# Kernel tuning notes

Measured on AMD Instinct MI355X. Metric: run time of the kernel, lower is better.

The kernel has to match this reference:

```python
import jax, jax.numpy as jnp
import numpy as np

EPS = 1e-6
D = 512      # embedding_dim
M = 4        # n_modules
B = 4        # batch
S = 128      # seq_len
K = 32       # stack_size
STEPS = 16   # max_steps (ACT)
SCALE = D ** (-0.5)


def _clin(zr, zi, Wr, Wi, sub):
    # complex linear: (Wr + i Wi)(zr + i zi), torch Linear convention y = x @ W.T
    yr = jnp.einsum(sub, zr, Wr) - jnp.einsum(sub, zi, Wi)
    yi = jnp.einsum(sub, zi, Wr) + jnp.einsum(sub, zr, Wi)
    return yr, yi


def forward_fn(x_real, x_imag, Wl_r, Wl_i, Wq_r, Wq_i, Wk_r, Wk_i, Wv_r, Wv_i,
               ln_scale, ln_shift, mod_bias, gate_mask,
               score_w, score_b, conf_w, conf_b, halt_w, halt_b,
               ctrl_w, ctrl_b, st_score_w, st_score_b, st_conf_w, st_conf_b):
    mem0 = jnp.zeros((B, K, 2 * D), x_real.dtype)
    ptr0 = jnp.zeros((B, K), x_real.dtype).at[:, 0].set(1.0)
    acc0 = jnp.zeros((B, S, 2 * D), x_real.dtype)
    rem0 = jnp.ones((B,), x_real.dtype)

    def step(carry, _):
        sr, si, mem, ptr, acc, rem = carry
        # ComplexAttentionBlock (all M modules vectorized on axis m)
        cr = 0.5 * x_real + 0.5 * sr
        ci = 0.5 * x_imag + 0.5 * si
        zr, zi = _clin(cr, ci, Wl_r, Wl_i, 'bsd,mod->bmso')   # [B,M,S,D]
        # ComplexLayerNorm (magnitude LN, unbiased var as torch.var default)
        mag = jnp.sqrt(zr * zr + zi * zi) + EPS
        mean = mag.mean(-1, keepdims=True)
        var = mag.var(-1, keepdims=True, ddof=1)
        nm = (mag - mean) / jnp.sqrt(var + EPS)
        nm = nm * ln_scale[None, :, None, :] + ln_shift[None, :, None, :]
        ph = jnp.arctan2(zi, zr)
        zr = nm * jnp.cos(ph)
        zi = nm * jnp.sin(ph)
        # ModReLU
        nrm = jnp.sqrt(zr * zr + zi * zi) + EPS
        sc = jax.nn.relu(nrm + mod_bias[None, :, None, :]) / nrm
        zr = zr * sc
        zi = zi * sc
        # ComplexAttention over concatenated real/imag q,k
        sub = 'bmsd,mod->bmso'
        qr, qi = _clin(zr, zi, Wq_r, Wq_i, sub)
        kr, ki = _clin(zr, zi, Wk_r, Wk_i, sub)
        vr, vi = _clin(zr, zi, Wv_r, Wv_i, sub)
        qf = jnp.concatenate([qr, qi], -1)   # [B,M,S,2D]
        kf = jnp.concatenate([kr, ki], -1)
        attn = jax.nn.softmax(jnp.einsum('bmse,bmte->bmst', qf, kf) * SCALE, axis=-1)
        ar = jnp.einsum('bmst,bmtd->bmsd', attn, vr)
        ai = jnp.einsum('bmst,bmtd->bmsd', attn, vi)
        # SigmoidGatingMask
        g = jax.nn.sigmoid(gate_mask)[None, :, None, :]
        pr = ar * g
        pi = ai * g
        flat = jnp.concatenate([pr, pi], -1)  # [B,M,S,2D]
        score = jnp.einsum('bmse,me->bms', flat, score_w) + score_b[None, :, None]
        conf = jax.nn.sigmoid(jnp.einsum('bmse,me->bms', flat, conf_w) + conf_b[None, :, None])
        halt = jnp.einsum('bmse,me->bms', flat, halt_w) + halt_b[None, :, None]
        # DifferentiableStack on seq-pooled broadcast state
        flat_in = jnp.concatenate([sr.mean(1), si.mean(1)], -1)  # [B,2D]
        control = jax.nn.softmax(flat_in @ ctrl_w + ctrl_b, axis=-1)  # [B,3]
        push, pop, noop = control[:, 0:1], control[:, 1:2], control[:, 2:3]
        ptr_up = jnp.roll(ptr, 1, axis=1)
        ptr_dn = jnp.roll(ptr, -1, axis=1)
        new_ptr = push * ptr_up + pop * ptr_dn + noop * ptr
        new_ptr = new_ptr / (new_ptr.sum(1, keepdims=True) + EPS)
        wmask = push * ptr_up                                   # [B,K]
        new_mem = wmask[..., None] * flat_in[:, None, :] + mem * (1.0 - wmask[..., None])
        read = (new_mem * new_ptr[..., None]).sum(1)            # [B,2D]
        sp_r, sp_i = read[:, :D], read[:, D:]
        st_sc = read @ st_score_w + st_score_b[0]               # [B]
        st_cf = jax.nn.sigmoid(read @ st_conf_w + st_conf_b[0])
        # combine M block proposals + stack proposal via score*confidence softmax
        all_pr = jnp.concatenate([pr, jnp.broadcast_to(sp_r[:, None, None, :], (B, 1, S, D))], 1)
        all_pi = jnp.concatenate([pi, jnp.broadcast_to(sp_i[:, None, None, :], (B, 1, S, D))], 1)
        all_sc = jnp.concatenate([score, jnp.broadcast_to(st_sc[:, None, None], (B, 1, S))], 1)
        all_cf = jnp.concatenate([conf, jnp.broadcast_to(st_cf[:, None, None], (B, 1, S))], 1)
        w = jax.nn.softmax(all_sc * all_cf, axis=1)[..., None]  # [B,M+1,S,1]
        new_sr = (w * all_pr).sum(1)
        new_si = (w * all_pi).sum(1)
        # ACT halting accumulation
        p = jax.nn.sigmoid(halt).mean(axis=(1, 2))              # [B]
        acc = acc + (p * rem)[:, None, None] * jnp.concatenate([new_sr, new_si], -1)
        rem = rem * (1.0 - p)
        return (new_sr, new_si, new_mem, new_ptr, acc, rem), None

    carry, _ = jax.lax.scan(step, (x_real, x_imag, mem0, ptr0, acc0, rem0), None, length=STEPS)
    sr, si, _, _, acc, rem = carry
    # add ACT remainder weight on final state
    out = acc + rem[:, None, None] * jnp.concatenate([sr, si], -1)
    return out  # [B,S,2D] real/imag concat


def setup_inputs() -> dict:
    key = jax.random.key(0)
    ks = jax.random.split(key, 24)
    w = 1.0 / np.sqrt(D)
    h = 0.02
    inp = {
        'x_real': jax.random.normal(ks[0], (B, S, D), jnp.float32),
        'x_imag': jax.random.normal(ks[1], (B, S, D), jnp.float32),
        'Wl_r': jax.random.normal(ks[2], (M, D, D), jnp.float32) * w,
        'Wl_i': jax.random.normal(ks[3], (M, D, D), jnp.float32) * w,
        'Wq_r': jax.random.normal(ks[4], (M, D, D), jnp.float32) * w,
        'Wq_i': jax.random.normal(ks[5], (M, D, D), jnp.float32) * w,
        'Wk_r': jax.random.normal(ks[6], (M, D, D), jnp.float32) * w,
        'Wk_i': jax.random.normal(ks[7], (M, D, D), jnp.float32) * w,
        'Wv_r': jax.random.normal(ks[8], (M, D, D), jnp.float32) * w,
        'Wv_i': jax.random.normal(ks[9], (M, D, D), jnp.float32) * w,
        'ln_scale': jnp.ones((M, D), jnp.float32),
        'ln_shift': jnp.zeros((M, D), jnp.float32),
        'mod_bias': jnp.zeros((M, D), jnp.float32),
        'gate_mask': jnp.ones((M, D), jnp.float32),
        'score_w': jax.random.normal(ks[10], (M, 2 * D), jnp.float32) * h,
        'score_b': jnp.zeros((M,), jnp.float32),
        'conf_w': jax.random.normal(ks[11], (M, 2 * D), jnp.float32) * h,
        'conf_b': jnp.zeros((M,), jnp.float32),
        'halt_w': jax.random.normal(ks[12], (M, 2 * D), jnp.float32) * h,
        'halt_b': jnp.full((M,), -4.0, jnp.float32),  # nn.init.constant_(halt_head.bias, -4.0)
        'ctrl_w': jax.random.normal(ks[13], (2 * D, 3), jnp.float32) * h,
        'ctrl_b': jnp.zeros((3,), jnp.float32),
        'st_score_w': jax.random.normal(ks[14], (2 * D,), jnp.float32) * h,
        'st_score_b': jnp.zeros((1,), jnp.float32),
        'st_conf_w': jax.random.normal(ks[15], (2 * D,), jnp.float32) * h,
        'st_conf_b': jnp.zeros((1,), jnp.float32),
    }
    return inp


def reference(x_real, x_imag, Wl_r, Wl_i, Wq_r, Wq_i, Wk_r, Wk_i, Wv_r, Wv_i,
              ln_scale, ln_shift, mod_bias, gate_mask,
              score_w, score_b, conf_w, conf_b, halt_w, halt_b,
              ctrl_w, ctrl_b, st_score_w, st_score_b, st_conf_w, st_conf_b):
    return forward_fn(x_real, x_imag, Wl_r, Wl_i, Wq_r, Wq_i, Wk_r, Wk_i, Wv_r, Wv_i,
                      ln_scale, ln_shift, mod_bias, gate_mask,
                      score_w, score_b, conf_w, conf_b, halt_w, halt_b,
                      ctrl_w, ctrl_b, st_score_w, st_score_b, st_conf_w, st_conf_b)
```

## Files before the change

kernel.cpp:

```cpp
#include <hip/hip_runtime.h>

#define DD 512
#define MM 4
#define BB 4
#define SS 128
#define KK 32
#define NSTEPS 16
#define EPSF 1e-6f
#define SCALEF 0.04419417382415922f
#define BMSD (BB * MM * SS * DD)

typedef unsigned short u16;
typedef __bf16 bf16x8 __attribute__((ext_vector_type(8)));
typedef u16 u16x8 __attribute__((ext_vector_type(8)));
typedef float f32x16 __attribute__((ext_vector_type(16)));
typedef unsigned int u32x4 __attribute__((ext_vector_type(4)));

__device__ inline void split_bf16(float x, u16& h, u16& l) {
  __bf16 hb = (__bf16)x;
  float hf = (float)hb;
  __bf16 lb = (__bf16)(x - hf);
  h = __builtin_bit_cast(u16, hb);
  l = __builtin_bit_cast(u16, lb);
}

__global__ void k_convw(const float* __restrict__ src, u16* __restrict__ dst) {
  int idx = blockIdx.x * 256 + threadIdx.x;
  int row = idx >> 9, k = idx & 511;
  u16 h, l;
  split_bf16(src[idx], h, l);
  dst[(size_t)row * 1024 + k] = h;
  dst[(size_t)row * 1024 + 512 + k] = l;
}

__global__ void k_convt(const float* __restrict__ src, u16* __restrict__ dst) {
  __shared__ float tile[64][65];
  int m = blockIdx.z;
  int o0 = blockIdx.y * 64, d0 = blockIdx.x * 64;
  int tid = threadIdx.x;
  int g = tid >> 6, lane = tid & 63;
#pragma unroll
  for (int i = 0; i < 16; i++) {
    int o_l = g * 16 + i;
    tile[o_l][lane] = src[(size_t)(m * 512 + o0 + o_l) * 512 + d0 + lane];
  }
  __syncthreads();
#pragma unroll
  for (int i = 0; i < 16; i++) {
    int d_l = g * 16 + i;
    float v = tile[lane][d_l];
    u16 h, l;
    split_bf16(v, h, l);
    size_t drow = (size_t)(m * 512 + d0 + d_l) * 1024;
    dst[drow + o0 + lane] = h;
    dst[drow + 512 + o0 + lane] = l;
  }
}

__global__ void k_init(const float* __restrict__ xr, const float* __restrict__ xi,
                       float* __restrict__ sr, float* __restrict__ si,
                       float* __restrict__ acc, float* __restrict__ memv,
                       float* __restrict__ ptrv, float* __restrict__ rem,
                       u16* __restrict__ crbf, u16* __restrict__ cibf) {
  int idx = blockIdx.x * 256 + threadIdx.x;
  if (idx < BB * SS * 2 * DD) acc[idx] = 0.f;
  if (idx < BB * SS * DD) {
    float a = xr[idx], b = xi[idx];
    sr[idx] = a; si[idx] = b;
    int row = idx >> 9, d = idx & 511;
    u16 h, l;
    split_bf16(a, h, l);
    crbf[(size_t)row * 1024 + d] = h;
    crbf[(size_t)row * 1024 + 512 + d] = l;
    split_bf16(b, h, l);
    cibf[(size_t)row * 1024 + d] = h;
    cibf[(size_t)row * 1024 + 512 + d] = l;
  }
  if (idx < BB * KK * 2 * DD) memv[idx] = 0.f;
  if (idx < BB * KK) ptrv[idx] = ((idx & (KK - 1)) == 0) ? 1.f : 0.f;
  if (idx < BB) rem[idx] = 1.f;
}

__global__ void k_flatctrl(const float* __restrict__ sr, const float* __restrict__ si,
                           const float* __restrict__ ctrl_w, const float* __restrict__ ctrl_b,
                           float* __restrict__ ptrv, float* __restrict__ flat_in,
                           float* __restrict__ nptrg, float* __restrict__ wmg,
                           float* __restrict__ stacc,
                           float* __restrict__ scorev, float* __restrict__ confv,
                           float* __restrict__ haltv) {
  int b = blockIdx.x;
  int tid = threadIdx.x;
  __shared__ float red[3 * 256];
  __shared__ float ctrl[3], optr[KK], nptr_s[KK], wm_s[KK], normf;

  if (tid < KK) optr[tid] = ptrv[b * KK + tid];

#pragma unroll
  for (int i = 0; i < 2; i++) {
    int r = b * MM * SS + tid + i * 256;
    scorev[r] = 0.f; confv[r] = 0.f; haltv[r] = 0.f;
  }

  int e4 = tid * 4;
  const float* basep = (e4 < DD) ? sr : si;
  int d4 = (e4 < DD) ? e4 : (e4 - DD);
  float4 accv = make_float4(0.f, 0.f, 0.f, 0.f);
  size_t base = (size_t)b * SS * DD + d4;
  for (int s = 0; s < SS; s++) {
    float4 v = *(const float4*)&basep[base + (size_t)s * DD];
    accv.x += v.x; accv.y += v.y; accv.z += v.z; accv.w += v.w;
  }
  accv.x *= (1.0f / SS); accv.y *= (1.0f / SS); accv.z *= (1.0f / SS); accv.w *= (1.0f / SS);
  *(float4*)&flat_in[b * 2 * DD + e4] = accv;
  float fv[4] = {accv.x, accv.y, accv.z, accv.w};
  float d0 = 0.f, d1 = 0.f, d2 = 0.f;
#pragma unroll
  for (int j = 0; j < 4; j++) {
    d0 += fv[j] * ctrl_w[(e4 + j) * 3 + 0];
    d1 += fv[j] * ctrl_w[(e4 + j) * 3 + 1];
    d2 += fv[j] * ctrl_w[(e4 + j) * 3 + 2];
  }
  red[tid] = d0; red[256 + tid] = d1; red[512 + tid] = d2;
  __syncthreads();
  for (int off = 128; off > 0; off >>= 1) {
    if (tid < off) {
      red[tid] += red[tid + off];
      red[256 + tid] += red[256 + tid + off];
      red[512 + tid] += red[512 + tid + off];
    }
    __syncthreads();
  }
  if (tid == 0) {
    float l0 = red[0] + ctrl_b[0], l1 = red[256] + ctrl_b[1], l2 = red[512] + ctrl_b[2];
    float mx = fmaxf(l0, fmaxf(l1, l2));
    float e0 = expf(l0 - mx), e1 = expf(l1 - mx), e2 = expf(l2 - mx);
    float s = e0 + e1 + e2;
    ctrl[0] = e0 / s; ctrl[1] = e1 / s; ctrl[2] = e2 / s;
    stacc[b * 2] = 0.f; stacc[b * 2 + 1] = 0.f;
  }
  __syncthreads();
  if (tid < KK) {
    float up = optr[(tid + KK - 1) & (KK - 1)];
    float dn = optr[(tid + 1) & (KK - 1)];
    float cu = optr[tid];
    nptr_s[tid] = ctrl[0] * up + ctrl[1] * dn + ctrl[2] * cu;
    wm_s[tid] = ctrl[0] * up;
  }
  __syncthreads();
  if (tid == 0) {
    float s = 0.f;
    for (int k = 0; k < KK; k++) s += nptr_s[k];
    normf = 1.f / (s + EPSF);
  }
  __syncthreads();
  if (tid < KK) {
    float np = nptr_s[tid] * normf;
    ptrv[b * KK + tid] = np;
    nptrg[b * KK + tid] = np;
    wmg[b * KK + tid] = wm_s[tid];
  }
}

#define LSTR 72

__global__ __launch_bounds__(256) void k_gemm_mfma(
    const u16* __restrict__ Ar, const u16* __restrict__ Ai,
    const u16* __restrict__ Wr, const u16* __restrict__ Wi,
    float* __restrict__ Cr, float* __restrict__ Ci) {
  __shared__ u16 sAr[64][LSTR], sAi[64][LSTR], sWr[64][LSTR], sWi[64][LSTR];
  int mz = blockIdx.z;
  int m = mz & (MM - 1), split = mz >> 2;
  int row_blk = blockIdx.y * 64, o_blk = blockIdx.x * 64;
  int tid = threadIdx.x;

  int lrow = tid >> 3, lk8 = (tid & 7) << 3;
  size_t arow0 = (size_t)(row_blk + lrow), arow1 = arow0 + 32;
  size_t wrow0 = (size_t)m * DD + o_blk + lrow, wrow1 = wrow0 + 32;

  int wave = tid >> 6, lane = tid & 63;
  int wrow = (wave >> 1) * 32, wcol = (wave & 1) * 32;
  int l31 = lane & 31, khalf = (lane >> 5) * 8;

  f32x16 accP, accN, accI;
  for (int i = 0; i < 16; i++) { accP[i] = 0.f; accN[i] = 0.f; accI[i] = 0.f; }

  {
    int it2 = split, seg = it2 >> 3, k0 = (it2 & 7) * 64;
    int aofs = (seg == 1) ? 512 : 0, wofs = (seg == 2) ? 512 : 0;
    (void)aofs; (void)wofs;
  }
  int it20 = split;
  int seg0 = it20 >> 3, k00 = (it20 & 7) * 64;
  int aofs0 = (seg0 == 1) ? 512 : 0, wofs0 = (seg0 == 2) ? 512 : 0;
  u16x8 g0 = *(const u16x8*)&Ar[arow0 * 1024 + aofs0 + k00 + lk8];
  u16x8 g1 = *(const u16x8*)&Ar[arow1 * 1024 + aofs0 + k00 + lk8];
  u16x8 g2 = *(const u16x8*)&Ai[arow0 * 1024 + aofs0 + k00 + lk8];
  u16x8 g3 = *(const u16x8*)&Ai[arow1 * 1024 + aofs0 + k00 + lk8];
  u16x8 g4 = *(const u16x8*)&Wr[wrow0 * 1024 + wofs0 + k00 + lk8];
  u16x8 g5 = *(const u16x8*)&Wr[wrow1 * 1024 + wofs0 + k00 + lk8];
  u16x8 g6 = *(const u16x8*)&Wi[wrow0 * 1024 + wofs0 + k00 + lk8];
  u16x8 g7 = *(const u16x8*)&Wi[wrow1 * 1024 + wofs0 + k00 + lk8];

  for (int jt = 0; jt < 12; ++jt) {
    __syncthreads();
    *(u16x8*)&sAr[lrow][lk8] = g0;
    *(u16x8*)&sAr[lrow + 32][lk8] = g1;
    *(u16x8*)&sAi[lrow][lk8] = g2;
    *(u16x8*)&sAi[lrow + 32][lk8] = g3;
    *(u16x8*)&sWr[lrow][lk8] = g4;
    *(u16x8*)&sWr[lrow + 32][lk8] = g5;
    *(u16x8*)&sWi[lrow][lk8] = g6;
    *(u16x8*)&sWi[lrow + 32][lk8] = g7;
    u16x8 n0, n1, n2, n3, n4, n5, n6, n7;
    if (jt < 11) {
      int it2 = 2 * (jt + 1) + split, seg = it2 >> 3, k0 = (it2 & 7) * 64;
      int aofs = (seg == 1) ? 512 : 0, wofs = (seg == 2) ? 512 : 0;
      n0 = *(const u16x8*)&Ar[arow0 * 1024 + aofs + k0 + lk8];
      n1 = *(const u16x8*)&Ar[arow1 * 1024 + aofs + k0 + lk8];
      n2 = *(const u16x8*)&Ai[arow0 * 1024 + aofs + k0 + lk8];
      n3 = *(const u16x8*)&Ai[arow1 * 1024 + aofs + k0 + lk8];
      n4 = *(const u16x8*)&Wr[wrow0 * 1024 + wofs + k0 + lk8];
      n5 = *(const u16x8*)&Wr[wrow1 * 1024 + wofs + k0 + lk8];
      n6 = *(const u16x8*)&Wi[wrow0 * 1024 + wofs + k0 + lk8];
      n7 = *(const u16x8*)&Wi[wrow1 * 1024 + wofs + k0 + lk8];
    }
    __syncthreads();
#pragma unroll
    for (int kk = 0; kk < 64; kk += 16) {
      bf16x8 fAr = *(const bf16x8*)&sAr[wrow + l31][kk + khalf];
      bf16x8 fAi = *(const bf16x8*)&sAi[wrow + l31][kk + khalf];
      bf16x8 fWr = *(const bf16x8*)&sWr[wcol + l31][kk + khalf];
      bf16x8 fWi = *(const bf16x8*)&sWi[wcol + l31][kk + khalf];
      accP = __builtin_amdgcn_mfma_f32_32x32x16_bf16(fAr, fWr, accP, 0, 0, 0);
      accN = __builtin_amdgcn_mfma_f32_32x32x16_bf16(fAi, fWi, accN, 0, 0, 0);
      accI = __builtin_amdgcn_mfma_f32_32x32x16_bf16(fAi, fWr, accI, 0, 0, 0);
      accI = __builtin_amdgcn_mfma_f32_32x32x16_bf16(fAr, fWi, accI, 0, 0, 0);
    }
    if (jt < 11) {
      g0 = n0; g1 = n1; g2 = n2; g3 = n3; g4 = n4; g5 = n5; g6 = n6; g7 = n7;
    }
  }

  int o = o_blk + wcol + l31;
  size_t sofs = (size_t)split * BMSD;
#pragma unroll
  for (int reg = 0; reg < 16; reg++) {
    int r_in = (reg & 3) + 8 * (reg >> 2) + 4 * (lane >> 5);
    int gr = row_blk + wrow + r_in;
    int b = gr >> 7, s = gr & (SS - 1);
    size_t crow = (size_t)((b * MM + m) * SS + s);
    Cr[sofs + crow * DD + o] = accP[reg] - accN[reg];
    Ci[sofs + crow * DD + o] = accI[reg];
  }
}

__global__ __launch_bounds__(256) void k_gemm_g(
    const u16* __restrict__ Ar, const u16* __restrict__ Ai,
    const u16* __restrict__ Wr, const u16* __restrict__ Wi,
    float* __restrict__ Hr, float* __restrict__ Hi) {
  __shared__ u16 sAr[64][LSTR], sAi[64][LSTR], sWr[64][LSTR], sWi[64][LSTR];
  int m = blockIdx.z;
  int row_blk = blockIdx.y * 64, o_blk = blockIdx.x * 64;
  int tid = threadIdx.x;

  int lrow = tid >> 3, lk8 = (tid & 7) << 3;
  size_t arow0 = (size_t)(m * 512 + row_blk + lrow), arow1 = arow0 + 32;
  size_t wrow0 = (size_t)(m * 512 + o_blk + lrow), wrow1 = wrow0 + 32;

  int wave = tid >> 6, lane = tid & 63;
  int wrow = (wave >> 1) * 32, wcol = (wave & 1) * 32;
  int l31 = lane & 31, khalf = (lane >> 5) * 8;

  f32x16 accP, accN, accI;
  for (int i = 0; i < 16; i++) { accP[i] = 0.f; accN[i] = 0.f; accI[i] = 0.f; }

  u16x8 g0 = *(const u16x8*)&Ar[arow0 * 1024 + lk8];
  u16x8 g1 = *(const u16x8*)&Ar[arow1 * 1024 + lk8];
  u16x8 g2 = *(const u16x8*)&Ai[arow0 * 1024 + lk8];
  u16x8 g3 = *(const u16x8*)&Ai[arow1 * 1024 + lk8];
  u16x8 g4 = *(const u16x8*)&Wr[wrow0 * 1024 + lk8];
  u16x8 g5 = *(const u16x8*)&Wr[wrow1 * 1024 + lk8];
  u16x8 g6 = *(const u16x8*)&Wi[wrow0 * 1024 + lk8];
  u16x8 g7 = *(const u16x8*)&Wi[wrow1 * 1024 + lk8];

  for (int it = 0; it < 24; ++it) {
    __syncthreads();
    *(u16x8*)&sAr[lrow][lk8] = g0;
    *(u16x8*)&sAr[lrow + 32][lk8] = g1;
    *(u16x8*)&sAi[lrow][lk8] = g2;
    *(u16x8*)&sAi[lrow + 32][lk8] = g3;
    *(u16x8*)&sWr[lrow][lk8] = g4;
    *(u16x8*)&sWr[lrow + 32][lk8] = g5;
    *(u16x8*)&sWi[lrow][lk8] = g6;
    *(u16x8*)&sWi[lrow + 32][lk8] = g7;
    u16x8 n0, n1, n2, n3, n4, n5, n6, n7;
    if (it < 23) {
      int it2 = it + 1, seg = it2 >> 3, k0 = (it2 & 7) * 64;
      int aofs = (seg == 1) ? 512 : 0, wofs = (seg == 2) ? 512 : 0;
      n0 = *(const u16x8*)&Ar[arow0 * 1024 + aofs + k0 + lk8];
      n1 = *(const u16x8*)&Ar[arow1 * 1024 + aofs + k0 + lk8];
      n2 = *(const u16x8*)&Ai[arow0 * 1024 + aofs + k0 + lk8];
      n3 = *(const u16x8*)&Ai[arow1 * 1024 + aofs + k0 + lk8];
      n4 = *(const u16x8*)&Wr[wrow0 * 1024 + wofs + k0 + lk8];
      n5 = *(const u16x8*)&Wr[wrow1 * 1024 + wofs + k0 + lk8];
      n6 = *(const u16x8*)&Wi[wrow0 * 1024 + wofs + k0 + lk8];
      n7 = *(const u16x8*)&Wi[wrow1 * 1024 + wofs + k0 + lk8];
    }
    __syncthreads();
#pragma unroll
    for (int kk = 0; kk < 64; kk += 16) {
      bf16x8 fAr = *(const bf16x8*)&sAr[wrow + l31][kk + khalf];
      bf16x8 fAi = *(const bf16x8*)&sAi[wrow + l31][kk + khalf];
      bf16x8 fWr = *(const bf16x8*)&sWr[wcol + l31][kk + khalf];
      bf16x8 fWi = *(const bf16x8*)&sWi[wcol + l31][kk + khalf];
      u32x4 t = __builtin_bit_cast(u32x4, fAi) ^ 0x80008000u;
      bf16x8 nAi = __builtin_bit_cast(bf16x8, t);
      accP = __builtin_amdgcn_mfma_f32_32x32x16_bf16(fAr, fWr, accP, 0, 0, 0);
      accN = __builtin_amdgcn_mfma_f32_32x32x16_bf16(fAi, fWi, accN, 0, 0, 0);
      accI = __builtin_amdgcn_mfma_f32_32x32x16_bf16(fAr, fWi, accI, 0, 0, 0);
      accI = __builtin_amdgcn_mfma_f32_32x32x16_bf16(nAi, fWr, accI, 0, 0, 0);
    }
    if (it < 23) {
      g0 = n0; g1 = n1; g2 = n2; g3 = n3; g4 = n4; g5 = n5; g6 = n6; g7 = n7;
    }
  }

  int o = o_blk + wcol + l31;
#pragma unroll
  for (int reg = 0; reg < 16; reg++) {
    int r_in = (reg & 3) + 8 * (reg >> 2) + 4 * (lane >> 5);
    int gr = row_blk + wrow + r_in;
    size_t crow = (size_t)(m * 512 + gr);
    Hr[crow * DD + o] = accP[reg] + accN[reg];
    Hi[crow * DD + o] = accI[reg];
  }
}

__global__ __launch_bounds__(256) void k_gemm_qkv(
    const u16* __restrict__ Ar, const u16* __restrict__ Ai,
    const u16* __restrict__ wbf, size_t WSLOT,
    u16* __restrict__ qbr, u16* __restrict__ qbi,
    u16* __restrict__ vbr, u16* __restrict__ vbi) {
  __shared__ u16 sAr[64][LSTR], sAi[64][LSTR], sWr[64][LSTR], sWi[64][LSTR];
// ... 195 lines not shown
  sum += __shfl_xor(sum, 2);
  float inv = 1.f / sum;
  size_t prow = (size_t)(bm * SS + s_blk + row) * 256;
#pragma unroll
  for (int j = 0; j < 32; j++) {
    int c = quarter * 32 + j;
    u16 h, l;
    split_bf16(ev[j] * inv, h, l);
    Pb[prow + c] = h;
    Pb[prow + 128 + c] = l;
  }
}

__global__ __launch_bounds__(256) void k_pv(
    const u16* __restrict__ Pb, const u16* __restrict__ vbr, const u16* __restrict__ vbi,
    const float* __restrict__ gate_mask,
    const float* __restrict__ score_w, const float* __restrict__ conf_w,
    const float* __restrict__ halt_w,
    float* __restrict__ pr, float* __restrict__ pi,
    float* __restrict__ scorev, float* __restrict__ confv, float* __restrict__ haltv) {
  __shared__ u16 sP[64][LSTR], sVr[64][LSTR], sVi[64][LSTR];
  int bm = blockIdx.z;
  int m = bm & (MM - 1);
  int s_blk = blockIdx.y * 64;
  int o_blk = blockIdx.x * 64;
  int tid = threadIdx.x;
  int lrow = tid >> 3, lk8 = (tid & 7) << 3;
  size_t prow0 = (size_t)(bm * SS + s_blk + lrow), prow1 = prow0 + 32;

  int wave = tid >> 6, lane = tid & 63;
  int wrow = (wave >> 1) * 32;
  int wcol = (wave & 1) * 32;
  int l31 = lane & 31, khalf = (lane >> 5) * 8;

  f32x16 accR, accI;
  for (int i = 0; i < 16; i++) { accR[i] = 0.f; accI[i] = 0.f; }

  for (int it = 0; it < 6; ++it) {
    int seg = it >> 1, k0 = (it & 1) * 64;
    int pofs = (seg == 1) ? 128 : 0;
    int vofs = (seg == 2) ? 512 : 0;
    u16x8 p0 = *(const u16x8*)&Pb[prow0 * 256 + pofs + k0 + lk8];
    u16x8 p1 = *(const u16x8*)&Pb[prow1 * 256 + pofs + k0 + lk8];
    size_t vrow0 = (size_t)(bm * SS + k0 + lrow), vrow1 = vrow0 + 32;
    u16x8 v0 = *(const u16x8*)&vbr[vrow0 * 1024 + vofs + o_blk + lk8];
    u16x8 v1 = *(const u16x8*)&vbr[vrow1 * 1024 + vofs + o_blk + lk8];
    u16x8 w0 = *(const u16x8*)&vbi[vrow0 * 1024 + vofs + o_blk + lk8];
    u16x8 w1 = *(const u16x8*)&vbi[vrow1 * 1024 + vofs + o_blk + lk8];
    __syncthreads();
    *(u16x8*)&sP[lrow][lk8] = p0;
    *(u16x8*)&sP[lrow + 32][lk8] = p1;
    *(u16x8*)&sVr[lrow][lk8] = v0;
    *(u16x8*)&sVr[lrow + 32][lk8] = v1;
    *(u16x8*)&sVi[lrow][lk8] = w0;
    *(u16x8*)&sVi[lrow + 32][lk8] = w1;
    __syncthreads();
#pragma unroll
    for (int kk = 0; kk < 64; kk += 16) {
      bf16x8 fP = *(const bf16x8*)&sP[wrow + l31][kk + khalf];
      u16x8 ar, ai;
#pragma unroll
      for (int j = 0; j < 8; j++) {
        ar[j] = sVr[kk + khalf + j][wcol + l31];
        ai[j] = sVi[kk + khalf + j][wcol + l31];
      }
      accR = __builtin_amdgcn_mfma_f32_32x32x16_bf16(fP, __builtin_bit_cast(bf16x8, ar), accR, 0, 0, 0);
      accI = __builtin_amdgcn_mfma_f32_32x32x16_bf16(fP, __builtin_bit_cast(bf16x8, ai), accI, 0, 0, 0);
    }
  }

  int d = o_blk + wcol + l31;
  float g = 1.f / (1.f + expf(-gate_mask[m * DD + d]));
  float swr = score_w[m * 2 * DD + d], swi = score_w[m * 2 * DD + DD + d];
  float cwr = conf_w[m * 2 * DD + d],  cwi = conf_w[m * 2 * DD + DD + d];
  float hwr = halt_w[m * 2 * DD + d],  hwi = halt_w[m * 2 * DD + DD + d];
#pragma unroll
  for (int reg = 0; reg < 16; reg++) {
    int r_in = (reg & 3) + 8 * (reg >> 2) + 4 * (lane >> 5);
    size_t crow = (size_t)(bm * SS + s_blk + wrow + r_in);
    float vR = accR[reg] * g, vI = accI[reg] * g;
    pr[crow * DD + d] = vR;
    pi[crow * DD + d] = vI;
    float ps = vR * swr + vI * swi;
    float pc = vR * cwr + vI * cwi;
    float ph = vR * hwr + vI * hwi;
#pragma unroll
    for (int off = 1; off < 32; off <<= 1) {
      ps += __shfl_xor(ps, off);
      pc += __shfl_xor(pc, off);
      ph += __shfl_xor(ph, off);
    }
    if (l31 == 0) {
      atomicAdd(&scorev[crow], ps);
      atomicAdd(&confv[crow], pc);
      atomicAdd(&haltv[crow], ph);
    }
  }
}

__global__ void k_lnphase(const float* __restrict__ zr, const float* __restrict__ zi,
                          const float* __restrict__ ln_scale, const float* __restrict__ ln_shift,
                          const float* __restrict__ mod_bias,
                          u16* __restrict__ zbr, u16* __restrict__ zbi) {
  int row = blockIdx.x;
  int m = (row >> 7) & (MM - 1);
  int tid = threadIdx.x;
  size_t base = (size_t)row * DD;
  float zrv[4], ziv[4], rv[4];
  float sum = 0.f, sumsq = 0.f;
#pragma unroll
  for (int i = 0; i < 4; i++) {
    int o = tid + i * 128;
    float a = zr[base + o] + zr[(size_t)BMSD + base + o];
    float bv = zi[base + o] + zi[(size_t)BMSD + base + o];
    zrv[i] = a; ziv[i] = bv;
    float r = sqrtf(a * a + bv * bv);
    rv[i] = r;
    float mg = r + EPSF;
    sum += mg;
    sumsq += mg * mg;
  }
  __shared__ float rs[128], rq[128];
  rs[tid] = sum; rq[tid] = sumsq;
  __syncthreads();
  for (int off = 64; off > 0; off >>= 1) {
    if (tid < off) { rs[tid] += rs[tid + off]; rq[tid] += rq[tid + off]; }
    __syncthreads();
  }
  float mean = rs[0] * (1.0f / DD);
  float var = (rq[0] - (float)DD * mean * mean) * (1.0f / (DD - 1));
  float inv = 1.0f / sqrtf(var + EPSF);
#pragma unroll
  for (int i = 0; i < 4; i++) {
    int o = tid + i * 128;
    float mg = rv[i] + EPSF;
    float nm = (mg - mean) * inv * ln_scale[m * DD + o] + ln_shift[m * DD + o];
    float r = rv[i];
    float cosp, sinp;
    if (r > 0.f) { cosp = zrv[i] / r; sinp = ziv[i] / r; }
    else { cosp = 1.f; sinp = 0.f; }
    float z1r = nm * cosp, z1i = nm * sinp;
    float nrm = sqrtf(z1r * z1r + z1i * z1i) + EPSF;
    float sc = fmaxf(nrm + mod_bias[m * DD + o], 0.f) / nrm;
    u16 h, l;
    split_bf16(z1r * sc, h, l);
    zbr[(size_t)row * 1024 + o] = h;
    zbr[(size_t)row * 1024 + 512 + o] = l;
    split_bf16(z1i * sc, h, l);
    zbi[(size_t)row * 1024 + o] = h;
    zbi[(size_t)row * 1024 + 512 + o] = l;
  }
}

__global__ void k_memup(const float* __restrict__ flat_in,
                        const float* __restrict__ nptrg, const float* __restrict__ wmg,
                        float* __restrict__ memv, float* __restrict__ readv,
                        const float* __restrict__ st_score_w, const float* __restrict__ st_conf_w,
                        float* __restrict__ stacc) {
  int b = blockIdx.x >> 2;
  int chunk = blockIdx.x & 3;
  int tid = threadIdx.x;
  int e = chunk * 256 + tid;
  __shared__ float nptr[KK], wm[KK];
  __shared__ float red[256], red2[256];
  if (tid < KK) { nptr[tid] = nptrg[b * KK + tid]; wm[tid] = wmg[b * KK + tid]; }
  __syncthreads();
  float fl = flat_in[b * 2 * DD + e];
  float racc = 0.f;
#pragma unroll
  for (int k = 0; k < KK; k++) {
    size_t idx = ((size_t)(b * KK + k)) * 2 * DD + e;
    float nm = wm[k] * fl + memv[idx] * (1.f - wm[k]);
    memv[idx] = nm;
    racc += nm * nptr[k];
  }
  readv[b * 2 * DD + e] = racc;
  red[tid] = racc * st_score_w[e];
  red2[tid] = racc * st_conf_w[e];
  __syncthreads();
  for (int off = 128; off > 0; off >>= 1) {
    if (tid < off) { red[tid] += red[tid + off]; red2[tid] += red2[tid + off]; }
    __syncthreads();
  }
  if (tid == 0) {
    atomicAdd(&stacc[b * 2], red[0]);
    atomicAdd(&stacc[b * 2 + 1], red2[0]);
  }
}

__global__ void k_haltp(const float* __restrict__ halt, const float* __restrict__ halt_b,
                        float* __restrict__ rem,
                        float* __restrict__ coeff, const float* __restrict__ stacc,
                        const float* __restrict__ st_score_b, const float* __restrict__ st_conf_b,
                        float* __restrict__ stv) {
  int b = blockIdx.x;
  int tid = threadIdx.x;
  __shared__ float red[256];
  float v0 = halt[b * MM * SS + tid] + halt_b[tid >> 7];
  float v1 = halt[b * MM * SS + 256 + tid] + halt_b[(tid + 256) >> 7];
  red[tid] = 1.f / (1.f + expf(-v0)) + 1.f / (1.f + expf(-v1));
  __syncthreads();
  for (int off = 128; off > 0; off >>= 1) {
    if (tid < off) red[tid] += red[tid + off];
    __syncthreads();
  }
  if (tid == 0) {
    float p = red[0] * (1.0f / (MM * SS));
    float r = rem[b];
    coeff[b] = p * r;
    rem[b] = r * (1.f - p);
    stv[b] = stacc[b * 2] + st_score_b[0];
    stv[BB + b] = 1.f / (1.f + expf(-(stacc[b * 2 + 1] + st_conf_b[0])));
  }
}

__global__ void k_combine(const float* __restrict__ pr, const float* __restrict__ pi,
                          const float* __restrict__ score, const float* __restrict__ conf,
                          const float* __restrict__ score_b, const float* __restrict__ conf_b,
                          const float* __restrict__ stv, const float* __restrict__ readv,
                          const float* __restrict__ coeff,
                          const float* __restrict__ xr, const float* __restrict__ xi,
                          float* __restrict__ sr, float* __restrict__ si, float* __restrict__ acc,
                          u16* __restrict__ crbf, u16* __restrict__ cibf) {
  int bs = blockIdx.x;
  int b = bs >> 7, s = bs & (SS - 1);
  int tid = threadIdx.x;
  __shared__ float w[5];
  if (tid == 0) {
    float l[5];
    for (int m = 0; m < MM; m++) {
      int r = (b * MM + m) * SS + s;
      float sc = score[r] + score_b[m];
      float cf = 1.f / (1.f + expf(-(conf[r] + conf_b[m])));
      l[m] = sc * cf;
    }
    l[4] = stv[b] * stv[BB + b];
    float mx = l[0];
    for (int j = 1; j < 5; j++) mx = fmaxf(mx, l[j]);
    float sum = 0.f;
    for (int j = 0; j < 5; j++) { l[j] = expf(l[j] - mx); sum += l[j]; }
    for (int j = 0; j < 5; j++) w[j] = l[j] / sum;
  }
  __syncthreads();
  float cf = coeff[b];
#pragma unroll
  for (int i = 0; i < 2; i++) {
    int d = tid + i * 256;
    float nsr = w[4] * readv[b * 2 * DD + d];
    float nsi = w[4] * readv[b * 2 * DD + DD + d];
#pragma unroll
    for (int m = 0; m < MM; m++) {
      size_t off = ((size_t)((b * MM + m) * SS + s)) * DD + d;
      nsr += w[m] * pr[off];
      nsi += w[m] * pi[off];
    }
    size_t sidx = (size_t)bs * DD + d;
    sr[sidx] = nsr;
    si[sidx] = nsi;
    size_t aoff = (size_t)bs * 2 * DD;
    acc[aoff + d] += cf * nsr;
    acc[aoff + DD + d] += cf * nsi;
    u16 h, l;
    split_bf16(0.5f * xr[sidx] + 0.5f * nsr, h, l);
    crbf[(size_t)bs * 1024 + d] = h;
    crbf[(size_t)bs * 1024 + 512 + d] = l;
    split_bf16(0.5f * xi[sidx] + 0.5f * nsi, h, l);
    cibf[(size_t)bs * 1024 + d] = h;
    cibf[(size_t)bs * 1024 + 512 + d] = l;
  }
}

__global__ void k_final(const float* __restrict__ acc, const float* __restrict__ rem,
                        const float* __restrict__ sr, const float* __restrict__ si,
                        float* __restrict__ out) {
  int idx = blockIdx.x * 256 + threadIdx.x;
  int e = idx & (2 * DD - 1);
  int bs = idx >> 10;
  int b = bs >> 7;
  float v = (e < DD) ? sr[(size_t)bs * DD + e] : si[(size_t)bs * DD + e - DD];
  out[idx] = acc[idx] + rem[b] * v;
}

extern "C" void kernel_launch(void* const* d_in, const int* in_sizes, int n_in,
                              void* d_out, int out_size, void* d_ws, size_t ws_size,
                              hipStream_t stream) {
  const float* xr = (const float*)d_in[0];
  const float* xi = (const float*)d_in[1];
  const float* Wl_r = (const float*)d_in[2];
  const float* Wl_i = (const float*)d_in[3];
  const float* Wq_r = (const float*)d_in[4];
  const float* Wq_i = (const float*)d_in[5];
  const float* Wk_r = (const float*)d_in[6];
  const float* Wk_i = (const float*)d_in[7];
  const float* Wv_r = (const float*)d_in[8];
  const float* Wv_i = (const float*)d_in[9];
  const float* ln_scale = (const float*)d_in[10];
  const float* ln_shift = (const float*)d_in[11];
  const float* mod_bias = (const float*)d_in[12];
  const float* gate_mask = (const float*)d_in[13];
  const float* score_w = (const float*)d_in[14];
  const float* score_b = (const float*)d_in[15];
  const float* conf_w = (const float*)d_in[16];
  const float* conf_b = (const float*)d_in[17];
  const float* halt_w = (const float*)d_in[18];
  const float* halt_b = (const float*)d_in[19];
  const float* ctrl_w = (const float*)d_in[20];
  const float* ctrl_b = (const float*)d_in[21];
  const float* st_score_w = (const float*)d_in[22];
  const float* st_score_b = (const float*)d_in[23];
  const float* st_conf_w = (const float*)d_in[24];
  const float* st_conf_b = (const float*)d_in[25];
  float* out = (float*)d_out;

  const int BSD = BB * SS * DD;
  const size_t WSLOT = (size_t)MM * DD * 1024;

  char* pc = (char*)d_ws;
  float* sr = (float*)pc; pc += (size_t)BSD * 4;
  float* si = (float*)pc; pc += (size_t)BSD * 4;
  float* zr = (float*)pc; pc += (size_t)2 * BMSD * 4;
  float* zi = (float*)pc; pc += (size_t)2 * BMSD * 4;
  float* prb = (float*)pc; pc += (size_t)BMSD * 4;
  float* pib = (float*)pc; pc += (size_t)BMSD * 4;
  float* scorev = (float*)pc; pc += (size_t)BB * MM * SS * 4;
  float* confv = (float*)pc; pc += (size_t)BB * MM * SS * 4;
  float* haltv = (float*)pc; pc += (size_t)BB * MM * SS * 4;
  float* flat = (float*)pc; pc += (size_t)BB * 2 * DD * 4;
  float* stacc = (float*)pc; pc += 64;
  float* nptrg = (float*)pc; pc += (size_t)BB * KK * 4;
  float* wmg = (float*)pc; pc += (size_t)BB * KK * 4;
  float* memv = (float*)pc; pc += (size_t)BB * KK * 2 * DD * 4;
  float* ptrv = (float*)pc; pc += (size_t)BB * KK * 4;
  float* readv = (float*)pc; pc += (size_t)BB * 2 * DD * 4;
  float* stv = (float*)pc; pc += (size_t)2 * BB * 4;
  float* accb = (float*)pc; pc += (size_t)BB * SS * 2 * DD * 4;
  float* rem = (float*)pc; pc += (size_t)BB * 4;
  float* coeff = (float*)pc; pc += (size_t)BB * 4;
  u16* crbf = (u16*)pc; pc += (size_t)BB * SS * 1024 * 2;
  u16* cibf = (u16*)pc; pc += (size_t)BB * SS * 1024 * 2;
  u16* zbr = (u16*)pc; pc += (size_t)BB * MM * SS * 1024 * 2;
  u16* zbi = (u16*)pc; pc += (size_t)BB * MM * SS * 1024 * 2;
  u16* qbr = (u16*)pc; pc += (size_t)BB * MM * SS * 1024 * 2;
  u16* qbi = (u16*)pc; pc += (size_t)BB * MM * SS * 1024 * 2;
  u16* vbr = (u16*)pc; pc += (size_t)BB * MM * SS * 1024 * 2;
  u16* vbi = (u16*)pc; pc += (size_t)BB * MM * SS * 1024 * 2;
  u16* Pb  = (u16*)pc; pc += (size_t)BB * MM * SS * 256 * 2;
  u16* wbf = (u16*)pc; pc += 10 * WSLOT * 2;
  u16* wqtr = (u16*)pc; pc += WSLOT * 2;
  u16* wqti = (u16*)pc; pc += WSLOT * 2;
  u16* wktr = (u16*)pc; pc += WSLOT * 2;
  u16* wkti = (u16*)pc; pc += WSLOT * 2;
  float* hfr = (float*)pc; pc += (size_t)MM * DD * DD * 4;
  float* hfi = (float*)pc; pc += (size_t)MM * DD * DD * 4;

  k_convw<<<4096, 256, 0, stream>>>(Wl_r, wbf + 0 * WSLOT);
  k_convw<<<4096, 256, 0, stream>>>(Wl_i, wbf + 1 * WSLOT);
  k_convw<<<4096, 256, 0, stream>>>(Wv_r, wbf + 6 * WSLOT);
  k_convw<<<4096, 256, 0, stream>>>(Wv_i, wbf + 7 * WSLOT);

  dim3 tgrid(8, 8, 4);
  k_convt<<<tgrid, 256, 0, stream>>>(Wq_r, wqtr);
  k_convt<<<tgrid, 256, 0, stream>>>(Wq_i, wqti);
  k_convt<<<tgrid, 256, 0, stream>>>(Wk_r, wktr);
  k_convt<<<tgrid, 256, 0, stream>>>(Wk_i, wkti);

  dim3 hgrid(8, 8, 4);
  k_gemm_g<<<hgrid, 256, 0, stream>>>(wktr, wkti, wqtr, wqti, hfr, hfi);
  k_convw<<<4096, 256, 0, stream>>>(hfr, wbf + 8 * WSLOT);
  k_convw<<<4096, 256, 0, stream>>>(hfi, wbf + 9 * WSLOT);

  k_init<<<2048, 256, 0, stream>>>(xr, xi, sr, si, accb, memv, ptrv, rem, crbf, cibf);

  dim3 ggrid(DD / 64, (BB * SS) / 64, MM * 2);
  dim3 qgrid(DD / 64, (BB * SS) / 64, MM * 2);
  dim3 smgrid(1, SS / 64, BB * MM);
  dim3 pvgrid(DD / 64, SS / 64, BB * MM);

  for (int step = 0; step < NSTEPS; ++step) {
    k_flatctrl<<<BB, 256, 0, stream>>>(sr, si, ctrl_w, ctrl_b, ptrv, flat, nptrg, wmg, stacc,
                                       scorev, confv, haltv);
    k_gemm_mfma<<<ggrid, 256, 0, stream>>>(crbf, cibf, wbf + 0 * WSLOT, wbf + 1 * WSLOT, zr, zi);
    k_lnphase<<<BB * MM * SS, 128, 0, stream>>>(zr, zi, ln_scale, ln_shift, mod_bias, zbr, zbi);
    k_gemm_qkv<<<qgrid, 256, 0, stream>>>(zbr, zbi, wbf, WSLOT, qbr, qbi, vbr, vbi);
    k_scores_sm<<<smgrid, 256, 0, stream>>>(qbr, qbi, zbr, zbi, Pb);
    k_pv<<<pvgrid, 256, 0, stream>>>(Pb, vbr, vbi, gate_mask, score_w, conf_w, halt_w,
                                     prb, pib, scorev, confv, haltv);
    k_memup<<<BB * 4, 256, 0, stream>>>(flat, nptrg, wmg, memv, readv,
                                        st_score_w, st_conf_w, stacc);
    k_haltp<<<BB, 256, 0, stream>>>(haltv, halt_b, rem, coeff, stacc, st_score_b, st_conf_b, stv);
    k_combine<<<BB * SS, 256, 0, stream>>>(prb, pib, scorev, confv, score_b, conf_b,
                                           stv, readv, coeff,
                                           xr, xi, sr, si, accb, crbf, cibf);
  }

  k_final<<<(BB * SS * 2 * DD) / 256, 256, 0, stream>>>(accb, rem, sr, si, out);
}
```

Baseline: 2.186 ms.

## Fuse stack controller, memory update and halting into fewer per-step kernels

Merges the flat/controller kernel with the stack memory update into one 512-thread kernel, and folds the halting-probability reduction into the combine kernel using ping-pong remainder buffers. The sequence-mean 'flat' vector is now accumulated with atomics inside combine and init instead of being re-read from sr/si each step. This cuts two kernel launches per step plus a pass over the state, at the cost of many global atomics in combine and redundant halt reductions in every combine block.

```diff
diff --git a/kernel.cpp b/kernel.cpp
--- a/kernel.cpp
+++ b/kernel.cpp
@@ -33,6 +33,10 @@
   dst[(size_t)row * 1024 + 512 + k] = l;
 }
 
+__global__ void k_zero(float* __restrict__ p) {
+  p[blockIdx.x * 256 + threadIdx.x] = 0.f;
+}
+
 __global__ void k_convt(const float* __restrict__ src, u16* __restrict__ dst) {
   __shared__ float tile[64][65];
   int m = blockIdx.z;
@@ -60,8 +64,9 @@
 __global__ void k_init(const float* __restrict__ xr, const float* __restrict__ xi,
                        float* __restrict__ sr, float* __restrict__ si,
                        float* __restrict__ acc, float* __restrict__ memv,
-                       float* __restrict__ ptrv, float* __restrict__ rem,
-                       u16* __restrict__ crbf, u16* __restrict__ cibf) {
+                       float* __restrict__ ptrv, float* __restrict__ rem2,
+                       u16* __restrict__ crbf, u16* __restrict__ cibf,
+                       float* __restrict__ flat) {
   int idx = blockIdx.x * 256 + threadIdx.x;
   if (idx < BB * SS * 2 * DD) acc[idx] = 0.f;
   if (idx < BB * SS * DD) {
@@ -75,75 +80,64 @@
     split_bf16(b, h, l);
     cibf[(size_t)row * 1024 + d] = h;
     cibf[(size_t)row * 1024 + 512 + d] = l;
+    int bb = idx >> 16;
+    atomicAdd(&flat[bb * 2 * DD + d], a * (1.0f / SS));
+    atomicAdd(&flat[bb * 2 * DD + DD + d], b * (1.0f / SS));
   }
   if (idx < BB * KK * 2 * DD) memv[idx] = 0.f;
   if (idx < BB * KK) ptrv[idx] = ((idx & (KK - 1)) == 0) ? 1.f : 0.f;
-  if (idx < BB) rem[idx] = 1.f;
-}
-
-__global__ void k_flatctrl(const float* __restrict__ sr, const float* __restrict__ si,
-                           const float* __restrict__ ctrl_w, const float* __restrict__ ctrl_b,
-                           float* __restrict__ ptrv, float* __restrict__ flat_in,
-                           float* __restrict__ nptrg, float* __restrict__ wmg,
-                           float* __restrict__ stacc,
-                           float* __restrict__ scorev, float* __restrict__ confv,
-                           float* __restrict__ haltv) {
+  if (idx < 2 * BB) rem2[idx] = 1.f;
+}
+
+__global__ __launch_bounds__(512) void k_stack(
+    float* __restrict__ flat,
+    const float* __restrict__ ctrl_w, const float* __restrict__ ctrl_b,
+    float* __restrict__ ptrv,
+    float* __restrict__ memv, float* __restrict__ readv,
+    const float* __restrict__ st_score_w, const float* __restrict__ st_conf_w,
+    const float* __restrict__ st_score_b, const float* __restrict__ st_conf_b,
+    float* __restrict__ stv,
+    float* __restrict__ scorev, float* __restrict__ confv, float* __restrict__ haltv) {
   int b = blockIdx.x;
   int tid = threadIdx.x;
-  __shared__ float red[3 * 256];
+  __shared__ float red[3 * 512];
   __shared__ float ctrl[3], optr[KK], nptr_s[KK], wm_s[KK], normf;
 
+  int hr = b * MM * SS + tid;
+  scorev[hr] = 0.f; confv[hr] = 0.f; haltv[hr] = 0.f;
+
   if (tid < KK) optr[tid] = ptrv[b * KK + tid];
 
-#pragma unroll
-  for (int i = 0; i < 2; i++) {
-    int r = b * MM * SS + tid + i * 256;
-    scorev[r] = 0.f; confv[r] = 0.f; haltv[r] = 0.f;
-  }
-
-  int e4 = tid * 4;
-  const float* basep = (e4 < DD) ? sr : si;
-  int d4 = (e4 < DD) ? e4 : (e4 - DD);
-  float4 accv = make_float4(0.f, 0.f, 0.f, 0.f);
-  size_t base = (size_t)b * SS * DD + d4;
-  for (int s = 0; s < SS; s++) {
-    float4 v = *(const float4*)&basep[base + (size_t)s * DD];
-    accv.x += v.x; accv.y += v.y; accv.z += v.z; accv.w += v.w;
-  }
-  accv.x *= (1.0f / SS); accv.y *= (1.0f / SS); accv.z *= (1.0f / SS); accv.w *= (1.0f / SS);
-  *(float4*)&flat_in[b * 2 * DD + e4] = accv;
-  float fv[4] = {accv.x, accv.y, accv.z, accv.w};
-  float d0 = 0.f, d1 = 0.f, d2 = 0.f;
-#pragma unroll
-  for (int j = 0; j < 4; j++) {
-    d0 += fv[j] * ctrl_w[(e4 + j) * 3 + 0];
-    d1 += fv[j] * ctrl_w[(e4 + j) * 3 + 1];
-    d2 += fv[j] * ctrl_w[(e4 + j) * 3 + 2];
-  }
-  red[tid] = d0; red[256 + tid] = d1; red[512 + tid] = d2;
-  __syncthreads();
-  for (int off = 128; off > 0; off >>= 1) {
+  float f0 = flat[b * 2 * DD + tid];
+  float f1 = flat[b * 2 * DD + 512 + tid];
+  flat[b * 2 * DD + tid] = 0.f;
+  flat[b * 2 * DD + 512 + tid] = 0.f;
+
+  float d0 = f0 * ctrl_w[tid * 3 + 0] + f1 * ctrl_w[(512 + tid) * 3 + 0];
+  float d1 = f0 * ctrl_w[tid * 3 + 1] + f1 * ctrl_w[(512 + tid) * 3 + 1];
+  float d2 = f0 * ctrl_w[tid * 3 + 2] + f1 * ctrl_w[(512 + tid) * 3 + 2];
+  red[tid] = d0; red[512 + tid] = d1; red[1024 + tid] = d2;
+  __syncthreads();
+  for (int off = 256; off > 0; off >>= 1) {
     if (tid < off) {
       red[tid] += red[tid + off];
-      red[256 + tid] += red[256 + tid + off];
       red[512 + tid] += red[512 + tid + off];
+      red[1024 + tid] += red[1024 + tid + off];
     }
     __syncthreads();
   }
   if (tid == 0) {
-    float l0 = red[0] + ctrl_b[0], l1 = red[256] + ctrl_b[1], l2 = red[512] + ctrl_b[2];
+    float l0 = red[0] + ctrl_b[0], l1 = red[512] + ctrl_b[1], l2 = red[1024] + ctrl_b[2];
     float mx = fmaxf(l0, fmaxf(l1, l2));
     float e0 = expf(l0 - mx), e1 = expf(l1 - mx), e2 = expf(l2 - mx);
     float s = e0 + e1 + e2;
     ctrl[0] = e0 / s; ctrl[1] = e1 / s; ctrl[2] = e2 / s;
-    stacc[b * 2] = 0.f; stacc[b * 2 + 1] = 0.f;
   }
   __syncthreads();
   if (tid < KK) {
     float up = optr[(tid + KK - 1) & (KK - 1)];
     float dn = optr[(tid + 1) & (KK - 1)];
-    float cu = optr[tid];
-    nptr_s[tid] = ctrl[0] * up + ctrl[1] * dn + ctrl[2] * cu;
+    nptr_s[tid] = ctrl[0] * up + ctrl[1] * dn + ctrl[2] * optr[tid];
     wm_s[tid] = ctrl[0] * up;
   }
   __syncthreads();
@@ -155,9 +149,35 @@
   __syncthreads();
   if (tid < KK) {
     float np = nptr_s[tid] * normf;
+    nptr_s[tid] = np;
     ptrv[b * KK + tid] = np;
-    nptrg[b * KK + tid] = np;
-    wmg[b * KK + tid] = wm_s[tid];
+  }
+  __syncthreads();
+
+  float racc0 = 0.f, racc1 = 0.f;
+#pragma unroll 4
+  for (int k = 0; k < KK; k++) {
+    size_t idx = ((size_t)(b * KK + k)) * 2 * DD;
+    float wmk = wm_s[k], np = nptr_s[k];
+    float m0 = memv[idx + tid], m1 = memv[idx + 512 + tid];
+    float n0 = wmk * f0 + m0 * (1.f - wmk);
+    float n1 = wmk * f1 + m1 * (1.f - wmk);
+    memv[idx + tid] = n0; memv[idx + 512 + tid] = n1;
+    racc0 += n0 * np; racc1 += n1 * np;
+  }
+  readv[b * 2 * DD + tid] = racc0;
+  readv[b * 2 * DD + 512 + tid] = racc1;
+  float rs = racc0 * st_score_w[tid] + racc1 * st_score_w[512 + tid];
+  float rc = racc0 * st_conf_w[tid] + racc1 * st_conf_w[512 + tid];
+  red[tid] = rs; red[512 + tid] = rc;
+  __syncthreads();
+  for (int off = 256; off > 0; off >>= 1) {
+    if (tid < off) { red[tid] += red[tid + off]; red[512 + tid] += red[512 + tid + off]; }
+    __syncthreads();
+  }
+  if (tid == 0) {
+    stv[b] = red[0] + st_score_b[0];
+    stv[BB + b] = 1.f / (1.f + expf(-(red[512] + st_conf_b[0])));
   }
 }
 
@@ -184,11 +204,6 @@
   f32x16 accP, accN, accI;
   for (int i = 0; i < 16; i++) { accP[i] = 0.f; accN[i] = 0.f; accI[i] = 0.f; }
 
-  {
-    int it2 = split, seg = it2 >> 3, k0 = (it2 & 7) * 64;
-    int aofs = (seg == 1) ? 512 : 0, wofs = (seg == 2) ? 512 : 0;
-    (void)aofs; (void)wofs;
-  }
   int it20 = split;
   int seg0 = it20 >> 3, k00 = (it20 & 7) * 64;
   int aofs0 = (seg0 == 1) ? 512 : 0, wofs0 = (seg0 == 2) ? 512 : 0;
@@ -690,87 +705,47 @@
   }
 }
 
-__global__ void k_memup(const float* __restrict__ flat_in,
-                        const float* __restrict__ nptrg, const float* __restrict__ wmg,
-                        float* __restrict__ memv, float* __restrict__ readv,
-                        const float* __restrict__ st_score_w, const float* __restrict__ st_conf_w,
-                        float* __restrict__ stacc) {
-  int b = blockIdx.x >> 2;
-  int chunk = blockIdx.x & 3;
-  int tid = threadIdx.x;
-  int e = chunk * 256 + tid;
-  __shared__ float nptr[KK], wm[KK];
-  __shared__ float red[256], red2[256];
-  if (tid < KK) { nptr[tid] = nptrg[b * KK + tid]; wm[tid] = wmg[b * KK + tid]; }
-  __syncthreads();
-  float fl = flat_in[b * 2 * DD + e];
-  float racc = 0.f;
-#pragma unroll
-  for (int k = 0; k < KK; k++) {
-    size_t idx = ((size_t)(b * KK + k)) * 2 * DD + e;
-    float nm = wm[k] * fl + memv[idx] * (1.f - wm[k]);
-    memv[idx] = nm;
-    racc += nm * nptr[k];
-  }
-  readv[b * 2 * DD + e] = racc;
-  red[tid] = racc * st_score_w[e];
-  red2[tid] = racc * st_conf_w[e];
-  __syncthreads();
-  for (int off = 128; off > 0; off >>= 1) {
-    if (tid < off) { red[tid] += red[tid + off]; red2[tid] += red2[tid + off]; }
-    __syncthreads();
-  }
-  if (tid == 0) {
-    atomicAdd(&stacc[b * 2], red[0]);
-    atomicAdd(&stacc[b * 2 + 1], red2[0]);
-  }
-}
-
-__global__ void k_haltp(const float* __restrict__ halt, const float* __restrict__ halt_b,
-                        float* __restrict__ rem,
-                        float* __restrict__ coeff, const float* __restrict__ stacc,
-                        const float* __restrict__ st_score_b, const float* __restrict__ st_conf_b,
-                        float* __restrict__ stv) {
-  int b = blockIdx.x;
-  int tid = threadIdx.x;
-  __shared__ float red[256];
-  float v0 = halt[b * MM * SS + tid] + halt_b[tid >> 7];
-  float v1 = halt[b * MM * SS + 256 + tid] + halt_b[(tid + 256) >> 7];
-  red[tid] = 1.f / (1.f + expf(-v0)) + 1.f / (1.f + expf(-v1));
-  __syncthreads();
-  for (int off = 128; off > 0; off >>= 1) {
-    if (tid < off) red[tid] += red[tid + off];
-    __syncthreads();
-  }
-  if (tid == 0) {
-    float p = red[0] * (1.0f / (MM * SS));
-    float r = rem[b];
-    coeff[b] = p * r;
-    rem[b] = r * (1.f - p);
-    stv[b] = stacc[b * 2] + st_score_b[0];
-    stv[BB + b] = 1.f / (1.f + expf(-(stacc[b * 2 + 1] + st_conf_b[0])));
-  }
-}
-
 __global__ void k_combine(const float* __restrict__ pr, const float* __restrict__ pi,
                           const float* __restrict__ score, const float* __restrict__ conf,
                           const float* __restrict__ score_b, const float* __restrict__ conf_b,
+                          const float* __restrict__ haltv, const float* __restrict__ halt_b,
                           const float* __restrict__ stv, const float* __restrict__ readv,
-                          const float* __restrict__ coeff,
+                          float* __restrict__ rem2, int parity,
                           const float* __restrict__ xr, const float* __restrict__ xi,
                           float* __restrict__ sr, float* __restrict__ si, float* __restrict__ acc,
-                          u16* __restrict__ crbf, u16* __restrict__ cibf) {
+                          u16* __restrict__ crbf, u16* __restrict__ cibf,
+                          float* __restrict__ flat) {
   int bs = blockIdx.x;
   int b = bs >> 7, s = bs & (SS - 1);
   int tid = threadIdx.x;
   __shared__ float w[5];
+  __shared__ float cf_s;
+  __shared__ float hred[256];
+
+  float hv = 0.f;
+#pragma unroll
+  for (int i = 0; i < 2; i++) {
+    int j = tid + i * 256;
+    float v = haltv[b * MM * SS + j] + halt_b[j >> 7];
+    hv += 1.f / (1.f + expf(-v));
+  }
+  hred[tid] = hv;
+  __syncthreads();
+  for (int off = 128; off > 0; off >>= 1) {
+    if (tid < off) hred[tid] += hred[tid + off];
+    __syncthreads();
+  }
   if (tid == 0) {
+    float p = hred[0] * (1.0f / (MM * SS));
+    float r = rem2[parity * BB + b];
+    cf_s = p * r;
+    if (s == 0) rem2[(parity ^ 1) * BB + b] = r * (1.f - p);
     float l[5];
     for (int m = 0; m < MM; m++) {
-      int r = (b * MM + m) * SS + s;
-      float sc = score[r] + score_b[m];
-      float cf = 1.f / (1.f + expf(-(conf[r] + conf_b[m])));
-      l[m] = sc * cf;
+      int rr = (b * MM + m) * SS + s;
+      float sc = score[rr] + score_b[m];
+      float cfd = 1.f / (1.f + expf(-(conf[rr] + conf_b[m])));
+      l[m] = sc * cfd;
     }
     l[4] = stv[b] * stv[BB + b];
     float mx = l[0];
@@ -780,7 +755,7 @@
     for (int j = 0; j < 5; j++) w[j] = l[j] / sum;
   }
   __syncthreads();
-  float cf = coeff[b];
+  float cf = cf_s;
 #pragma unroll
   for (int i = 0; i < 2; i++) {
     int d = tid + i * 256;
@@ -805,6 +780,8 @@
     split_bf16(0.5f * xi[sidx] + 0.5f * nsi, h, l);
     cibf[(size_t)bs * 1024 + d] = h;
     cibf[(size_t)bs * 1024 + 512 + d] = l;
+    atomicAdd(&flat[b * 2 * DD + d], nsr * (1.0f / SS));
+    atomicAdd(&flat[b * 2 * DD + DD + d], nsi * (1.0f / SS));
   }
 }
 
@@ -864,16 +841,12 @@
   float* confv = (float*)pc; pc += (size_t)BB * MM * SS * 4;
   float* haltv = (float*)pc; pc += (size_t)BB * MM * SS * 4;
   float* flat = (float*)pc; pc += (size_t)BB * 2 * DD * 4;
-  float* stacc = (float*)pc; pc += 64;
-  float* nptrg = (float*)pc; pc += (size_t)BB * KK * 4;
-  float* wmg = (float*)pc; pc += (size_t)BB * KK * 4;
   float* memv = (float*)pc; pc += (size_t)BB * KK * 2 * DD * 4;
   float* ptrv = (float*)pc; pc += (size_t)BB * KK * 4;
   float* readv = (float*)pc; pc += (size_t)BB * 2 * DD * 4;
   float* stv = (float*)pc; pc += (size_t)2 * BB * 4;
   float* accb = (float*)pc; pc += (size_t)BB * SS * 2 * DD * 4;
-  float* rem = (float*)pc; pc += (size_t)BB * 4;
-  float* coeff = (float*)pc; pc += (size_t)BB * 4;
+  float* rem2 = (float*)pc; pc += (size_t)2 * BB * 4;
   u16* crbf = (u16*)pc; pc += (size_t)BB * SS * 1024 * 2;
   u16* cibf = (u16*)pc; pc += (size_t)BB * SS * 1024 * 2;
   u16* zbr = (u16*)pc; pc += (size_t)BB * MM * SS * 1024 * 2;
@@ -891,6 +864,7 @@
   float* hfr = (float*)pc; pc += (size_t)MM * DD * DD * 4;
   float* hfi = (float*)pc; pc += (size_t)MM * DD * DD * 4;
 
+  k_zero<<<(BB * 2 * DD) / 256, 256, 0, stream>>>(flat);
   k_convw<<<4096, 256, 0, stream>>>(Wl_r, wbf + 0 * WSLOT);
   k_convw<<<4096, 256, 0, stream>>>(Wl_i, wbf + 1 * WSLOT);
   k_convw<<<4096, 256, 0, stream>>>(Wv_r, wbf + 6 * WSLOT);
@@ -907,7 +881,7 @@
   k_convw<<<4096, 256, 0, stream>>>(hfr, wbf + 8 * WSLOT);
   k_convw<<<4096, 256, 0, stream>>>(hfi, wbf + 9 * WSLOT);
 
-  k_init<<<2048, 256, 0, stream>>>(xr, xi, sr, si, accb, memv, ptrv, rem, crbf, cibf);
+  k_init<<<2048, 256, 0, stream>>>(xr, xi, sr, si, accb, memv, ptrv, rem2, crbf, cibf, flat);
 
   dim3 ggrid(DD / 64, (BB * SS) / 64, MM * 2);
   dim3 qgrid(DD / 64, (BB * SS) / 64, MM * 2);
@@ -915,21 +889,19 @@
   dim3 pvgrid(DD / 64, SS / 64, BB * MM);
 
   for (int step = 0; step < NSTEPS; ++step) {
-    k_flatctrl<<<BB, 256, 0, stream>>>(sr, si, ctrl_w, ctrl_b, ptrv, flat, nptrg, wmg, stacc,
-                                       scorev, confv, haltv);
+    k_stack<<<BB, 512, 0, stream>>>(flat, ctrl_w, ctrl_b, ptrv, memv, readv,
+                                    st_score_w, st_conf_w, st_score_b, st_conf_b,
+                                    stv, scorev, confv, haltv);
     k_gemm_mfma<<<ggrid, 256, 0, stream>>>(crbf, cibf, wbf + 0 * WSLOT, wbf + 1 * WSLOT, zr, zi);
     k_lnphase<<<BB * MM * SS, 128, 0, stream>>>(zr, zi, ln_scale, ln_shift, mod_bias, zbr, zbi);
     k_gemm_qkv<<<qgrid, 256, 0, stream>>>(zbr, zbi, wbf, WSLOT, qbr, qbi, vbr, vbi);
     k_scores_sm<<<smgrid, 256, 0, stream>>>(qbr, qbi, zbr, zbi, Pb);
     k_pv<<<pvgrid, 256, 0, stream>>>(Pb, vbr, vbi, gate_mask, score_w, conf_w, halt_w,
                                      prb, pib, scorev, confv, haltv);
-    k_memup<<<BB * 4, 256, 0, stream>>>(flat, nptrg, wmg, memv, readv,
-                                        st_score_w, st_conf_w, stacc);
-    k_haltp<<<BB, 256, 0, stream>>>(haltv, halt_b, rem, coeff, stacc, st_score_b, st_conf_b, stv);
     k_combine<<<BB * SS, 256, 0, stream>>>(prb, pib, scorev, confv, score_b, conf_b,
-                                           stv, readv, coeff,
-                                           xr, xi, sr, si, accb, crbf, cibf);
-  }
-
-  k_final<<<(BB * SS * 2 * DD) / 256, 256, 0, stream>>>(accb, rem, sr, si, out);
-}
+                                           haltv, halt_b, stv, readv, rem2, step & 1,
+                                           xr, xi, sr, si, accb, crbf, cibf, flat);
+  }
+
+  k_final<<<(BB * SS * 2 * DD) / 256, 256, 0, stream>>>(accb, rem2, sr, si, out);
+}
```

After: 2.270 ms. +3.9%, slower.
